# Kernel tuning notes

Hardware: AMD Instinct MI355X
Metric: run time of the kernel (lower is better)

Reference implementation:

```python
import jax, jax.numpy as jnp
import numpy as np

IN_NF, IN_EF, OUT_NF, H1, H2, H_IN = 16, 8, 16, 8, 8, 16
N_NODES, N_EDGES = 100000, 2000000


def _mlp(x, w1, b1, w2, b2):
    # Linear -> LeakyReLU(0.2) -> Linear
    return jax.nn.leaky_relu(x @ w1 + b1, negative_slope=0.2) @ w2 + b2


def setup_inputs() -> dict:
    key = jax.random.key(0)
    ks = jax.random.split(key, 20)
    d_in = 2 * IN_NF + IN_EF  # 40
    inp = {
        "nf": jax.random.normal(ks[0], (N_NODES, IN_NF), jnp.float32),
        "src_out": jax.random.randint(ks[1], (N_EDGES,), 0, N_NODES),
        "dst_out": jax.random.randint(ks[2], (N_EDGES,), 0, N_NODES),
        "nef_out": jax.random.normal(ks[3], (N_EDGES, IN_EF), jnp.float32),
        "src_in": jax.random.randint(ks[4], (N_EDGES,), 0, N_NODES),
        "dst_in": jax.random.randint(ks[5], (N_EDGES,), 0, N_NODES),
        "nef_in": jax.random.normal(ks[6], (N_EDGES, IN_EF), jnp.float32),
        # MLP_msg_o2i: (2*in_nf+in_ef) -> h_in -> out_nf
        "w_o2i1": jax.random.normal(ks[7], (d_in, H_IN), jnp.float32) * 0.1,
        "b_o2i1": jnp.zeros((H_IN,), jnp.float32),
        "w_o2i2": jax.random.normal(ks[8], (H_IN, OUT_NF), jnp.float32) * 0.1,
        "b_o2i2": jnp.zeros((OUT_NF,), jnp.float32),
        # MLP_msg_i2o: (2*in_nf+in_ef) -> h_in -> 1+h1+h2
        "w_i2o1": jax.random.normal(ks[9], (d_in, H_IN), jnp.float32) * 0.1,
        "b_i2o1": jnp.zeros((H_IN,), jnp.float32),
        "w_i2o2": jax.random.normal(ks[10], (H_IN, 1 + H1 + H2), jnp.float32) * 0.1,
        "b_i2o2": jnp.zeros((1 + H1 + H2,), jnp.float32),
        # MLP_reduce_o: (in_nf+h1+h2) -> h_in -> out_nf  (note: in_nf==out_nf here)
        "w_red1": jax.random.normal(ks[11], (OUT_NF + H1 + H2, H_IN), jnp.float32) * 0.1,
        "b_red1": jnp.zeros((H_IN,), jnp.float32),
        "w_red2": jax.random.normal(ks[12], (H_IN, OUT_NF), jnp.float32) * 0.1,
        "b_red2": jnp.zeros((OUT_NF,), jnp.float32),
    }
    return inp


def reference(nf, src_out, dst_out, nef_out, src_in, dst_in, nef_in,
              w_o2i1, b_o2i1, w_o2i2, b_o2i2,
              w_i2o1, b_i2o1, w_i2o2, b_i2o2,
              w_red1, b_red1, w_red2, b_red2):
    n = nf.shape[0]
    # --- update_all over 'net_out': edge gather-concat -> MLP -> scatter sum
    x_o = jnp.concatenate([nf[src_out], nf[dst_out], nef_out], axis=1)  # [E, 40]
    efi = _mlp(x_o, w_o2i1, b_o2i1, w_o2i2, b_o2i2)                      # [E, out_nf]
    new_nf = jax.ops.segment_sum(efi, dst_out, num_segments=n)           # overwrites 'new_nf'
    # --- apply_edges over 'net_in': gated messages
    x_i = jnp.concatenate([nf[src_in], nf[dst_in], nef_in], axis=1)      # [E, 40]
    m = _mlp(x_i, w_i2o1, b_i2o1, w_i2o2, b_i2o2)                        # [E, 1+h1+h2]
    k = jax.nn.sigmoid(m[:, :1])
    efo1 = m[:, 1:1 + H1] * k
    efo2 = m[:, 1 + H1:] * k
    # --- scatter sum / mean into dst nodes
    nfo1 = jax.ops.segment_sum(efo1, dst_in, num_segments=n)
    cnt = jax.ops.segment_sum(jnp.ones((dst_in.shape[0],), nf.dtype), dst_in, num_segments=n)
    nfo2 = jax.ops.segment_sum(efo2, dst_in, num_segments=n) / jnp.maximum(cnt, 1.0)[:, None]
    # --- apply_nodes only on net_in destination nodes; others keep new_nf
    reduced = _mlp(jnp.concatenate([new_nf, nfo1, nfo2], axis=1), w_red1, b_red1, w_red2, b_red2)
    has_in = (cnt > 0)[:, None]
    return jnp.where(has_in, reduced, new_nf)
```

## Files before the change

### kernel.cpp

```cpp
#include <hip/hip_runtime.h>
#include <math.h>

#define IN_NF 16
#define IN_EF 8
#define OUT_NF 16
#define H1 8
#define H2 8
#define H_IN 16
#define NT 4
#define SCAN_NB 128

typedef unsigned int uivec4 __attribute__((ext_vector_type(4)));

__device__ __forceinline__ unsigned int f2bf_bits(float f) {
    unsigned int u = __float_as_uint(f);
    u += 0x7FFFu + ((u >> 16) & 1u);
    return u >> 16;
}
__device__ __forceinline__ float bf_lo(unsigned int w) { return __uint_as_float(w << 16); }
__device__ __forceinline__ float bf_hi(unsigned int w) { return __uint_as_float(w & 0xFFFF0000u); }

__global__ __launch_bounds__(256) void k_pre(
    const float* __restrict__ nf, unsigned short* __restrict__ nf16, int n_nodes,
    const int* __restrict__ dst_out, const int* __restrict__ dst_in,
// ... 20 lines not shown
            atomicAdd(&curA[a.x], 1); atomicAdd(&curA[a.y], 1);
            atomicAdd(&curA[a.z], 1); atomicAdd(&curA[a.w], 1);
            int4 b = *(const int4*)(dst_in + i);
            atomicAdd(&curB[b.x], 1); atomicAdd(&curB[b.y], 1);
            atomicAdd(&curB[b.z], 1); atomicAdd(&curB[b.w], 1);
        } else {
            for (int e = i; e < n_edges; ++e) {
                atomicAdd(&curA[dst_out[e]], 1);
                atomicAdd(&curB[dst_in[e]], 1);
            }
        }
    }
}

__global__ __launch_bounds__(256) void k_scan_partial(
    const int* __restrict__ a0, const int* __restrict__ a1, int n,
    int* __restrict__ bsum)
{
    int arr = blockIdx.x >> 7;
    int blk = blockIdx.x & (SCAN_NB - 1);
    const int* a = arr ? a1 : a0;
    int chunk = (n + SCAN_NB - 1) / SCAN_NB;
    int beg = blk * chunk;
    int end = min(beg + chunk, n);
    int s = 0;
    for (int i = beg + threadIdx.x; i < end; i += 256) s += a[i];
    __shared__ int sm[256];
    int t = threadIdx.x;
    sm[t] = s;
    __syncthreads();
    for (int d = 128; d > 0; d >>= 1) {
        if (t < d) sm[t] += sm[t + d];
        __syncthreads();
    }
    if (t == 0) bsum[arr * SCAN_NB + blk] = sm[0];
}

__global__ __launch_bounds__(64) void k_scan_bsum(int* __restrict__ bsum)
{
    int arr = threadIdx.x;
    if (arr >= 2) return;
    int run = 0;
    for (int i = 0; i < SCAN_NB; ++i) {
        int v = bsum[arr * SCAN_NB + i];
        bsum[arr * SCAN_NB + i] = run;
        run += v;
    }
}

__global__ __launch_bounds__(256) void k_scan_final(
    int* __restrict__ a0, int* __restrict__ a1, int n,
    const int* __restrict__ bsum)
{
    int arr = blockIdx.x >> 7;
    int blk = blockIdx.x & (SCAN_NB - 1);
    int* a = arr ? a1 : a0;
    int chunk = (n + SCAN_NB - 1) / SCAN_NB;
    int beg = blk * chunk;
    int end = min(beg + chunk, n);
    int t = threadIdx.x;
    __shared__ int sm[256];
    __shared__ int carry_sm;
    if (t == 0) carry_sm = bsum[arr * SCAN_NB + blk];
    __syncthreads();
    for (int base = beg; base < end; base += 256) {
        int i = base + t;
        int v = (i < end) ? a[i] : 0;
        sm[t] = v;
        __syncthreads();
        for (int d = 1; d < 256; d <<= 1) {
            int u = (t >= d) ? sm[t - d] : 0;
            __syncthreads();
            sm[t] += u;
            __syncthreads();
        }
        int carry = carry_sm;
        if (i < end) a[i] = carry + sm[t] - v;
        __syncthreads();
        if (t == 0) carry_sm = carry + sm[255];
        __syncthreads();
    }
}

__global__ __launch_bounds__(256, 4) void k_edges_stream(
    const unsigned short* __restrict__ nf16,
    const int* __restrict__ srcA, const int* __restrict__ dstA,
    const float* __restrict__ nefA,
    const int* __restrict__ srcB, const int* __restrict__ dstB,
    const float* __restrict__ nefB,
    const float* __restrict__ W1A, const float* __restrict__ B1A,
    const float* __restrict__ W2A, const float* __restrict__ B2A,
    const float* __restrict__ W1B, const float* __restrict__ B1B,
    const float* __restrict__ W2B, const float* __restrict__ B2B,
    int* __restrict__ curA, int* __restrict__ curB,
    int* __restrict__ invA, int* __restrict__ invB,
    unsigned short* __restrict__ msgA, unsigned short* __restrict__ msgB,
    int n_edges, int nbe)
{
    bool isA = (int)blockIdx.x < nbe;
    int bid = isA ? (int)blockIdx.x : (int)blockIdx.x - nbe;
    int e = bid * 256 + (int)threadIdx.x;
    if (e >= n_edges) return;

    const int* src = isA ? srcA : srcB;
    const int* dst = isA ? dstA : dstB;
    const float* nef = isA ? nefA : nefB;
    const float* W1 = isA ? W1A : W1B;
    const float* B1 = isA ? B1A : B1B;
    int* cursor = isA ? curA : curB;
    int* inv = isA ? invA : invB;
    unsigned short* msg = isA ? msgA : msgB;

    int s = src[e];
    int d = dst[e];

    const uint4* pS = (const uint4*)(nf16 + (size_t)s * 16);
    uint4 Sa = pS[0], Sb = pS[1];
    const uint4* pD = (const uint4*)(nf16 + (size_t)d * 16);
    uint4 Da = pD[0], Db = pD[1];
    const float4* pN = (const float4*)(nef + (size_t)e * IN_EF);
    float4 Na = pN[0], Nb = pN[1];

    int slot = atomicAdd(&cursor[d], 1);

    float h[H_IN];
#pragma unroll
    for (int j = 0; j < H_IN; ++j) h[j] = B1[j];
    {
        unsigned int wS[8] = {Sa.x,Sa.y,Sa.z,Sa.w,Sb.x,Sb.y,Sb.z,Sb.w};
        unsigned int wD[8] = {Da.x,Da.y,Da.z,Da.w,Db.x,Db.y,Db.z,Db.w};
#pragma unroll
        for (int w = 0; w < 8; ++w) {
            float a0 = bf_lo(wS[w]), a1 = bf_hi(wS[w]);
            float b0 = bf_lo(wD[w]), b1 = bf_hi(wD[w]);
            const float* r0 = W1 + (2*w) * H_IN;
            const float* r1 = W1 + (2*w+1) * H_IN;
            const float* r2 = W1 + (IN_NF + 2*w) * H_IN;
            const float* r3 = W1 + (IN_NF + 2*w+1) * H_IN;
#pragma unroll
            for (int j = 0; j < H_IN; ++j) {
                h[j] = fmaf(a0, r0[j], h[j]);
                h[j] = fmaf(a1, r1[j], h[j]);
                h[j] = fmaf(b0, r2[j], h[j]);
                h[j] = fmaf(b1, r3[j], h[j]);
            }
        }
        float nv[8] = {Na.x,Na.y,Na.z,Na.w,Nb.x,Nb.y,Nb.z,Nb.w};
#pragma unroll
        for (int k = 0; k < IN_EF; ++k) {
            const float* r = W1 + (2*IN_NF + k) * H_IN;
            float a0 = nv[k];
#pragma unroll
            for (int j = 0; j < H_IN; ++j) h[j] = fmaf(a0, r[j], h[j]);
        }
    }
#pragma unroll
    for (int j = 0; j < H_IN; ++j) h[j] = (h[j] >= 0.f) ? h[j] : 0.2f * h[j];

    unsigned int w[8];
    if (isA) {
        float o[OUT_NF];
#pragma unroll
        for (int j = 0; j < OUT_NF; ++j) o[j] = B2A[j];
#pragma unroll
        for (int k = 0; k < H_IN; ++k) {
            float hk = h[k];
            const float* r = W2A + k * OUT_NF;
#pragma unroll
            for (int j = 0; j < OUT_NF; ++j) o[j] = fmaf(hk, r[j], o[j]);
        }
#pragma unroll
        for (int q = 0; q < 8; ++q)
            w[q] = f2bf_bits(o[2*q]) | (f2bf_bits(o[2*q+1]) << 16);
    } else {
        const int M = 1 + H1 + H2;
        float o[17];
#pragma unroll
        for (int j = 0; j < M; ++j) o[j] = B2B[j];
#pragma unroll
        for (int k = 0; k < H_IN; ++k) {
            float hk = h[k];
            const float* r = W2B + k * M;
#pragma unroll
            for (int j = 0; j < M; ++j) o[j] = fmaf(hk, r[j], o[j]);
        }
        float g = 1.f / (1.f + __expf(-o[0]));
#pragma unroll
        for (int q = 0; q < 8; ++q)
            w[q] = f2bf_bits(o[1+2*q] * g) | (f2bf_bits(o[2+2*q] * g) << 16);
    }

    uivec4* pm = (uivec4*)(msg + (size_t)e * 16);
    uivec4 v0 = {w[0], w[1], w[2], w[3]};
    uivec4 v1 = {w[4], w[5], w[6], w[7]};
    __builtin_nontemporal_store(v0, pm);
    __builtin_nontemporal_store(v1, pm + 1);
    inv[slot] = e;
}

__global__ __launch_bounds__(256, 4) void k_gather_ind(
    const int* __restrict__ curA, const int* __restrict__ curB,
    const int* __restrict__ invA, const int* __restrict__ invB,
    const unsigned short* __restrict__ msgA, const unsigned short* __restrict__ msgB,
    const float* __restrict__ w_red1, const float* __restrict__ b_red1,
    const float* __restrict__ w_red2, const float* __restrict__ b_red2,
    float* __restrict__ out, int n_nodes)
{
    int tid = blockIdx.x * blockDim.x + threadIdx.x;
    int node = tid >> 2;
    int t = tid & (NT - 1);
    if (node >= n_nodes) return;

    int begA = (node == 0) ? 0 : curA[node - 1];
    int endA = curA[node];
    int begB = (node == 0) ? 0 : curB[node - 1];
    int endB = curB[node];

    float accA[16], accB[16];
#pragma unroll
    for (int j = 0; j < 16; ++j) { accA[j] = 0.f; accB[j] = 0.f; }

    {
        int i = begA + t;
        int e = (i < endA) ? invA[i] : 0;
        while (i < endA) {
            int inext = i + NT;
            int enext = (inext < endA) ? invA[inext] : 0;
            const uint4* p = (const uint4*)(msgA + (size_t)e * 16);
            uint4 v0 = p[0], v1 = p[1];
            unsigned int w0=v0.x,w1=v0.y,w2=v0.z,w3=v0.w,w4=v1.x,w5=v1.y,w6=v1.z,w7=v1.w;
            accA[0]+=bf_lo(w0); accA[1]+=bf_hi(w0); accA[2]+=bf_lo(w1); accA[3]+=bf_hi(w1);
            accA[4]+=bf_lo(w2); accA[5]+=bf_hi(w2); accA[6]+=bf_lo(w3); accA[7]+=bf_hi(w3);
            accA[8]+=bf_lo(w4); accA[9]+=bf_hi(w4); accA[10]+=bf_lo(w5); accA[11]+=bf_hi(w5);
            accA[12]+=bf_lo(w6); accA[13]+=bf_hi(w6); accA[14]+=bf_lo(w7); accA[15]+=bf_hi(w7);
            i = inext; e = enext;
        }
    }
    {
        int i = begB + t;
        int e = (i < endB) ? invB[i] : 0;
        while (i < endB) {
            int inext = i + NT;
            int enext = (inext < endB) ? invB[inext] : 0;
            const uint4* p = (const uint4*)(msgB + (size_t)e * 16);
            uint4 v0 = p[0], v1 = p[1];
            unsigned int w0=v0.x,w1=v0.y,w2=v0.z,w3=v0.w,w4=v1.x,w5=v1.y,w6=v1.z,w7=v1.w;
            accB[0]+=bf_lo(w0); accB[1]+=bf_hi(w0); accB[2]+=bf_lo(w1); accB[3]+=bf_hi(w1);
            accB[4]+=bf_lo(w2); accB[5]+=bf_hi(w2); accB[6]+=bf_lo(w3); accB[7]+=bf_hi(w3);
            accB[8]+=bf_lo(w4); accB[9]+=bf_hi(w4); accB[10]+=bf_lo(w5); accB[11]+=bf_hi(w5);
            accB[12]+=bf_lo(w6); accB[13]+=bf_hi(w6); accB[14]+=bf_lo(w7); accB[15]+=bf_hi(w7);
            i = inext; e = enext;
        }
    }

#pragma unroll
    for (int mask = 1; mask < NT; mask <<= 1) {
#pragma unroll
        for (int j = 0; j < 16; ++j) {
            accA[j] += __shfl_xor(accA[j], mask);
            accB[j] += __shfl_xor(accB[j], mask);
        }
    }
    if (t != 0) return;

    int deg = endB - begB;
    float inv = 1.f / fmaxf((float)deg, 1.f);
    float x2[32];
#pragma unroll
    for (int j = 0; j < 16; ++j) x2[j] = accA[j];
#pragma unroll
    for (int j = 0; j < H1; ++j) x2[16 + j] = accB[j];
#pragma unroll
    for (int j = 0; j < H2; ++j) x2[16 + H1 + j] = accB[8 + j] * inv;

    float h[H_IN];
#pragma unroll
    for (int j = 0; j < H_IN; ++j) h[j] = b_red1[j];
#pragma unroll
    for (int k = 0; k < 32; ++k) {
        float xk = x2[k];
#pragma unroll
        for (int j = 0; j < H_IN; ++j) h[j] = fmaf(xk, w_red1[k * H_IN + j], h[j]);
    }
#pragma unroll
    for (int j = 0; j < H_IN; ++j) h[j] = (h[j] >= 0.f) ? h[j] : 0.2f * h[j];

    float o[OUT_NF];
#pragma unroll
    for (int j = 0; j < OUT_NF; ++j) o[j] = b_red2[j];
#pragma unroll
    for (int k = 0; k < H_IN; ++k) {
        float hk = h[k];
#pragma unroll
        for (int j = 0; j < OUT_NF; ++j) o[j] = fmaf(hk, w_red2[k * OUT_NF + j], o[j]);
    }

    bool has_in = (deg > 0);
    float4* po = (float4*)(out + (long)node * OUT_NF);
#pragma unroll
    for (int i = 0; i < 4; ++i) {
        float4 v;
        if (has_in) { v.x=o[4*i+0]; v.y=o[4*i+1]; v.z=o[4*i+2]; v.w=o[4*i+3]; }
        else        { v.x=accA[4*i+0]; v.y=accA[4*i+1]; v.z=accA[4*i+2]; v.w=accA[4*i+3]; }
        po[i] = v;
    }
}

__global__ __launch_bounds__(256, 4) void k_edges_csr(
    const unsigned short* __restrict__ nf16,
    const int* __restrict__ srcA, const int* __restrict__ dstA,
    const float* __restrict__ nefA,
    const int* __restrict__ srcB, const int* __restrict__ dstB,
    const float* __restrict__ nefB,
    const float* __restrict__ W1A, const float* __restrict__ B1A,
    const float* __restrict__ W2A, const float* __restrict__ B2A,
    const float* __restrict__ W1B, const float* __restrict__ B1B,
    const float* __restrict__ W2B, const float* __restrict__ B2B,
    int* __restrict__ curA, int* __restrict__ curB,
    unsigned short* __restrict__ msgA, unsigned short* __restrict__ msgB,
    int n_edges, int nbe)
{
    bool isA = (int)blockIdx.x < nbe;
    int bid = isA ? (int)blockIdx.x : (int)blockIdx.x - nbe;
    int e = bid * 256 + (int)threadIdx.x;
    if (e >= n_edges) return;

    const int* src = isA ? srcA : srcB;
    const int* dst = isA ? dstA : dstB;
    const float* nef = isA ? nefA : nefB;
    const float* W1 = isA ? W1A : W1B;
    const float* B1 = isA ? B1A : B1B;
    int* cursor = isA ? curA : curB;
    unsigned short* msg = isA ? msgA : msgB;

    int s = src[e];
    int d = dst[e];

    const uint4* pS = (const uint4*)(nf16 + (size_t)s * 16);
    uint4 Sa = pS[0], Sb = pS[1];
    const uint4* pD = (const uint4*)(nf16 + (size_t)d * 16);
    uint4 Da = pD[0], Db = pD[1];
    const float4* pN = (const float4*)(nef + (size_t)e * IN_EF);
    float4 Na = pN[0], Nb = pN[1];

    int slot = atomicAdd(&cursor[d], 1);

    float h[H_IN];
#pragma unroll
    for (int j = 0; j < H_IN; ++j) h[j] = B1[j];
    {
        unsigned int wS[8] = {Sa.x,Sa.y,Sa.z,Sa.w,Sb.x,Sb.y,Sb.z,Sb.w};
        unsigned int wD[8] = {Da.x,Da.y,Da.z,Da.w,Db.x,Db.y,Db.z,Db.w};
#pragma unroll
        for (int w = 0; w < 8; ++w) {
            float a0 = bf_lo(wS[w]), a1 = bf_hi(wS[w]);
            float b0 = bf_lo(wD[w]), b1 = bf_hi(wD[w]);
            const float* r0 = W1 + (2*w) * H_IN;
            const float* r1 = W1 + (2*w+1) * H_IN;
            const float* r2 = W1 + (IN_NF + 2*w) * H_IN;
            const float* r3 = W1 + (IN_NF + 2*w+1) * H_IN;
#pragma unroll
            for (int j = 0; j < H_IN; ++j) {
                h[j] = fmaf(a0, r0[j], h[j]);
                h[j] = fmaf(a1, r1[j], h[j]);
                h[j] = fmaf(b0, r2[j], h[j]);
                h[j] = fmaf(b1, r3[j], h[j]);
            }
        }
        float nv[8] = {Na.x,Na.y,Na.z,Na.w,Nb.x,Nb.y,Nb.z,Nb.w};
#pragma unroll
        for (int k = 0; k < IN_EF; ++k) {
            const float* r = W1 + (2*IN_NF + k) * H_IN;
            float a0 = nv[k];
#pragma unroll
            for (int j = 0; j < H_IN; ++j) h[j] = fmaf(a0, r[j], h[j]);
        }
    }
#pragma unroll
    for (int j = 0; j < H_IN; ++j) h[j] = (h[j] >= 0.f) ? h[j] : 0.2f * h[j];

    unsigned int w[8];
    if (isA) {
        float o[OUT_NF];
#pragma unroll
        for (int j = 0; j < OUT_NF; ++j) o[j] = B2A[j];
#pragma unroll
        for (int k = 0; k < H_IN; ++k) {
            float hk = h[k];
            const float* r = W2A + k * OUT_NF;
#pragma unroll
            for (int j = 0; j < OUT_NF; ++j) o[j] = fmaf(hk, r[j], o[j]);
        }
#pragma unroll
        for (int q = 0; q < 8; ++q)
            w[q] = f2bf_bits(o[2*q]) | (f2bf_bits(o[2*q+1]) << 16);
    } else {
        const int M = 1 + H1 + H2;
        float o[17];
#pragma unroll
        for (int j = 0; j < M; ++j) o[j] = B2B[j];
#pragma unroll
        for (int k = 0; k < H_IN; ++k) {
            float hk = h[k];
            const float* r = W2B + k * M;
#pragma unroll
            for (int j = 0; j < M; ++j) o[j] = fmaf(hk, r[j], o[j]);
        }
        float g = 1.f / (1.f + __expf(-o[0]));
#pragma unroll
        for (int q = 0; q < 8; ++q)
            w[q] = f2bf_bits(o[1+2*q] * g) | (f2bf_bits(o[2+2*q] * g) << 16);
    }

    uivec4* pm = (uivec4*)(msg + (size_t)slot * 16);
    uivec4 v0 = {w[0], w[1], w[2], w[3]};
    uivec4 v1 = {w[4], w[5], w[6], w[7]};
    __builtin_nontemporal_store(v0, pm);
    __builtin_nontemporal_store(v1, pm + 1);
}

__global__ __launch_bounds__(256, 4) void k_gather_csr(
    const int* __restrict__ curA, const int* __restrict__ curB,
    const unsigned short* __restrict__ msgA, const unsigned short* __restrict__ msgB,
    const float* __restrict__ w_red1, const float* __restrict__ b_red1,
    const float* __restrict__ w_red2, const float* __restrict__ b_red2,
    float* __restrict__ out, int n_nodes)
{
    int tid = blockIdx.x * blockDim.x + threadIdx.x;
    int node = tid >> 2;
    int t = tid & (NT - 1);
    if (node >= n_nodes) return;

    int begA = (node == 0) ? 0 : curA[node - 1];
    int endA = curA[node];
    int begB = (node == 0) ? 0 : curB[node - 1];
    int endB = curB[node];

    float accA[16], accB[16];
#pragma unroll
    for (int j = 0; j < 16; ++j) { accA[j] = 0.f; accB[j] = 0.f; }

    for (int i = begA + t; i < endA; i += NT) {
        const uint4* p = (const uint4*)(msgA + (size_t)i * 16);
        uint4 v0 = p[0], v1 = p[1];
        unsigned int w0=v0.x,w1=v0.y,w2=v0.z,w3=v0.w,w4=v1.x,w5=v1.y,w6=v1.z,w7=v1.w;
        accA[0]+=bf_lo(w0); accA[1]+=bf_hi(w0); accA[2]+=bf_lo(w1); accA[3]+=bf_hi(w1);
        accA[4]+=bf_lo(w2); accA[5]+=bf_hi(w2); accA[6]+=bf_lo(w3); accA[7]+=bf_hi(w3);
        accA[8]+=bf_lo(w4); accA[9]+=bf_hi(w4); accA[10]+=bf_lo(w5); accA[11]+=bf_hi(w5);
        accA[12]+=bf_lo(w6); accA[13]+=bf_hi(w6); accA[14]+=bf_lo(w7); accA[15]+=bf_hi(w7);
    }
    for (int i = begB + t; i < endB; i += NT) {
        const uint4* p = (const uint4*)(msgB + (size_t)i * 16);
        uint4 v0 = p[0], v1 = p[1];
        unsigned int w0=v0.x,w1=v0.y,w2=v0.z,w3=v0.w,w4=v1.x,w5=v1.y,w6=v1.z,w7=v1.w;
        accB[0]+=bf_lo(w0); accB[1]+=bf_hi(w0); accB[2]+=bf_lo(w1); accB[3]+=bf_hi(w1);
        accB[4]+=bf_lo(w2); accB[5]+=bf_hi(w2); accB[6]+=bf_lo(w3); accB[7]+=bf_hi(w3);
        accB[8]+=bf_lo(w4); accB[9]+=bf_hi(w4); accB[10]+=bf_lo(w5); accB[11]+=bf_hi(w5);
        accB[12]+=bf_lo(w6); accB[13]+=bf_hi(w6); accB[14]+=bf_lo(w7); accB[15]+=bf_hi(w7);
    }

#pragma unroll
    for (int mask = 1; mask < NT; mask <<= 1) {
#pragma unroll
        for (int j = 0; j < 16; ++j) {
            accA[j] += __shfl_xor(accA[j], mask);
            accB[j] += __shfl_xor(accB[j], mask);
        }
    }
    if (t != 0) return;

    int deg = endB - begB;
    float inv = 1.f / fmaxf((float)deg, 1.f);
    float x2[32];
#pragma unroll
    for (int j = 0; j < 16; ++j) x2[j] = accA[j];
#pragma unroll
    for (int j = 0; j < H1; ++j) x2[16 + j] = accB[j];
#pragma unroll
    for (int j = 0; j < H2; ++j) x2[16 + H1 + j] = accB[8 + j] * inv;

    float h[H_IN];
#pragma unroll
    for (int j = 0; j < H_IN; ++j) h[j] = b_red1[j];
#pragma unroll
    for (int k = 0; k < 32; ++k) {
        float xk = x2[k];
#pragma unroll
        for (int j = 0; j < H_IN; ++j) h[j] = fmaf(xk, w_red1[k * H_IN + j], h[j]);
    }
#pragma unroll
    for (int j = 0; j < H_IN; ++j) h[j] = (h[j] >= 0.f) ? h[j] : 0.2f * h[j];

    float o[OUT_NF];
#pragma unroll
    for (int j = 0; j < OUT_NF; ++j) o[j] = b_red2[j];
#pragma unroll
    for (int k = 0; k < H_IN; ++k) {
        float hk = h[k];
#pragma unroll
        for (int j = 0; j < OUT_NF; ++j) o[j] = fmaf(hk, w_red2[k * OUT_NF + j], o[j]);
    }

    bool has_in = (deg > 0);
    float4* po = (float4*)(out + (long)node * OUT_NF);
#pragma unroll
    for (int i = 0; i < 4; ++i) {
        float4 v;
        if (has_in) { v.x=o[4*i+0]; v.y=o[4*i+1]; v.z=o[4*i+2]; v.w=o[4*i+3]; }
        else        { v.x=accA[4*i+0]; v.y=accA[4*i+1]; v.z=accA[4*i+2]; v.w=accA[4*i+3]; }
        po[i] = v;
    }
}

extern "C" void kernel_launch(void* const* d_in, const int* in_sizes, int n_in,
                              void* d_out, int out_size, void* d_ws, size_t ws_size,
                              hipStream_t stream) {
    const float* nf      = (const float*)d_in[0];
    const int*   src_out = (const int*)d_in[1];
    const int*   dst_out = (const int*)d_in[2];
    const float* nef_out = (const float*)d_in[3];
    const int*   src_in  = (const int*)d_in[4];
    const int*   dst_in  = (const int*)d_in[5];
    const float* nef_in  = (const float*)d_in[6];
    const float* w_o2i1  = (const float*)d_in[7];
    const float* b_o2i1  = (const float*)d_in[8];
    const float* w_o2i2  = (const float*)d_in[9];
    const float* b_o2i2  = (const float*)d_in[10];
    const float* w_i2o1  = (const float*)d_in[11];
    const float* b_i2o1  = (const float*)d_in[12];
    const float* w_i2o2  = (const float*)d_in[13];
    const float* b_i2o2  = (const float*)d_in[14];
    const float* w_red1  = (const float*)d_in[15];
    const float* b_red1  = (const float*)d_in[16];
    const float* w_red2  = (const float*)d_in[17];
    const float* b_red2  = (const float*)d_in[18];

    int n_nodes = in_sizes[0] / IN_NF;
    int n_edges = in_sizes[1];
    float* out = (float*)d_out;

    dim3 blk(256);
    dim3 ngrid(((size_t)n_nodes * NT + 255) / 256);
    dim3 sgrid(2 * SCAN_NB);

    size_t off_bytes  = (size_t)2 * n_nodes * sizeof(int);
    size_t nf16_bytes = (size_t)n_nodes * 16 * sizeof(unsigned short);
    size_t inv_bytes  = (size_t)n_edges * sizeof(int);
    size_t msg_bytes  = (size_t)n_edges * 16 * sizeof(unsigned short);
    size_t need2 = off_bytes + nf16_bytes + 2 * inv_bytes + 2 * msg_bytes + 256;

    int nb_conv = (n_nodes + 255) / 256;
    int nb_hist = (n_edges / 4 + 256) / 256 + 1;
    dim3 pgrid(nb_conv + nb_hist);
    int nbe = (n_edges + 255) / 256;
    dim3 edge_grid(2 * nbe);

    if (ws_size >= need2) {
        int* curA = (int*)d_ws;
        int* curB = curA + n_nodes;
        unsigned short* nf16 = (unsigned short*)(curB + n_nodes);
        int* invA = (int*)(nf16 + (size_t)n_nodes * 16);
        int* invB = invA + n_edges;
        unsigned short* msgA = (unsigned short*)(invB + n_edges);
        unsigned short* msgB = msgA + (size_t)n_edges * 16;
        int* bsum = (int*)msgA;

        hipMemsetAsync(d_ws, 0, off_bytes, stream);
        k_pre<<<pgrid, blk, 0, stream>>>(nf, nf16, n_nodes, dst_out, dst_in,
                                         curA, curB, n_edges, nb_conv);
        k_scan_partial<<<sgrid, blk, 0, stream>>>(curA, curB, n_nodes, bsum);
        k_scan_bsum<<<dim3(1), dim3(64), 0, stream>>>(bsum);
        k_scan_final<<<sgrid, blk, 0, stream>>>(curA, curB, n_nodes, bsum);
        k_edges_stream<<<edge_grid, blk, 0, stream>>>(nf16,
                                               src_out, dst_out, nef_out,
                                               src_in, dst_in, nef_in,
                                               w_o2i1, b_o2i1, w_o2i2, b_o2i2,
                                               w_i2o1, b_i2o1, w_i2o2, b_i2o2,
                                               curA, curB, invA, invB,
                                               msgA, msgB, n_edges, nbe);
        k_gather_ind<<<ngrid, blk, 0, stream>>>(curA, curB, invA, invB,
                                            msgA, msgB,
                                            w_red1, b_red1, w_red2, b_red2,
                                            out, n_nodes);
    } else {
        int* curA = (int*)d_ws;
        int* curB = curA + n_nodes;
        unsigned short* nf16 = (unsigned short*)(curB + n_nodes);
        unsigned short* msgA = nf16 + (size_t)n_nodes * 16;
        unsigned short* msgB = msgA + (size_t)n_edges * 16;
        int* bsum = (int*)msgA;

        hipMemsetAsync(d_ws, 0, off_bytes, stream);
        k_pre<<<pgrid, blk, 0, stream>>>(nf, nf16, n_nodes, dst_out, dst_in,
                                         curA, curB, n_edges, nb_conv);
        k_scan_partial<<<sgrid, blk, 0, stream>>>(curA, curB, n_nodes, bsum);
        k_scan_bsum<<<dim3(1), dim3(64), 0, stream>>>(bsum);
        k_scan_final<<<sgrid, blk, 0, stream>>>(curA, curB, n_nodes, bsum);
        k_edges_csr<<<edge_grid, blk, 0, stream>>>(nf16,
                                               src_out, dst_out, nef_out,
                                               src_in, dst_in, nef_in,
                                               w_o2i1, b_o2i1, w_o2i2, b_o2i2,
                                               w_i2o1, b_i2o1, w_i2o2, b_i2o2,
                                               curA, curB, msgA, msgB,
                                               n_edges, nbe);
        k_gather_csr<<<ngrid, blk, 0, stream>>>(curA, curB, msgA, msgB,
                                            w_red1, b_red1, w_red2, b_red2,
                                            out, n_nodes);
    }
}
```

Before: 566.8 us.

## Compute edge MLPs per destination node, skipping per-edge message buffers

Replaces the edge-parallel MLP pass, which wrote bf16 messages for a later gather, with a lightweight permutation scatter followed by destination-node kernels. These walk each node's incoming edges, run the MLPs in place and accumulate the results directly. The destination-node part of the first layer and the second-layer bias are hoisted out of the per-edge loop. This removes the per-edge message write and reread, at the cost of random reads of src features and nef through the permutation and load imbalance across node degrees. The fallback path for small workspaces is dropped.

```diff
diff --git a/kernel.cpp b/kernel.cpp
--- a/kernel.cpp
+++ b/kernel.cpp
@@ -126,289 +126,85 @@
     }
 }
 
-__global__ __launch_bounds__(256, 4) void k_edges_stream(
+__global__ __launch_bounds__(256) void k_scatter(
+    const int* __restrict__ dst_out, const int* __restrict__ dst_in,
+    int* __restrict__ curA, int* __restrict__ curB,
+    int* __restrict__ permA, int* __restrict__ permB, int n_edges)
+{
+    int e = blockIdx.x * blockDim.x + threadIdx.x;
+    if (e >= n_edges) return;
+    int p0 = atomicAdd(&curA[dst_out[e]], 1);
+    permA[p0] = e;
+    int p1 = atomicAdd(&curB[dst_in[e]], 1);
+    permB[p1] = e;
+}
+
+__global__ __launch_bounds__(256, 4) void k_nodeA(
     const unsigned short* __restrict__ nf16,
-    const int* __restrict__ srcA, const int* __restrict__ dstA,
-    const float* __restrict__ nefA,
-    const int* __restrict__ srcB, const int* __restrict__ dstB,
-    const float* __restrict__ nefB,
-    const float* __restrict__ W1A, const float* __restrict__ B1A,
-    const float* __restrict__ W2A, const float* __restrict__ B2A,
-    const float* __restrict__ W1B, const float* __restrict__ B1B,
-    const float* __restrict__ W2B, const float* __restrict__ B2B,
-    int* __restrict__ curA, int* __restrict__ curB,
-    int* __restrict__ invA, int* __restrict__ invB,
-    unsigned short* __restrict__ msgA, unsigned short* __restrict__ msgB,
-    int n_edges, int nbe)
-{
-    bool isA = (int)blockIdx.x < nbe;
-    int bid = isA ? (int)blockIdx.x : (int)blockIdx.x - nbe;
-    int e = bid * 256 + (int)threadIdx.x;
-    if (e >= n_edges) return;
-
-    const int* src = isA ? srcA : srcB;
-    const int* dst = isA ? dstA : dstB;
-    const float* nef = isA ? nefA : nefB;
-    const float* W1 = isA ? W1A : W1B;
-    const float* B1 = isA ? B1A : B1B;
-    int* cursor = isA ? curA : curB;
-    int* inv = isA ? invA : invB;
-    unsigned short* msg = isA ? msgA : msgB;
-
-    int s = src[e];
-    int d = dst[e];
-
-    const uint4* pS = (const uint4*)(nf16 + (size_t)s * 16);
-    uint4 Sa = pS[0], Sb = pS[1];
-    const uint4* pD = (const uint4*)(nf16 + (size_t)d * 16);
-    uint4 Da = pD[0], Db = pD[1];
-    const float4* pN = (const float4*)(nef + (size_t)e * IN_EF);
-    float4 Na = pN[0], Nb = pN[1];
-
-    int slot = atomicAdd(&cursor[d], 1);
-
-    float h[H_IN];
-#pragma unroll
-    for (int j = 0; j < H_IN; ++j) h[j] = B1[j];
-    {
-        unsigned int wS[8] = {Sa.x,Sa.y,Sa.z,Sa.w,Sb.x,Sb.y,Sb.z,Sb.w};
-        unsigned int wD[8] = {Da.x,Da.y,Da.z,Da.w,Db.x,Db.y,Db.z,Db.w};
-#pragma unroll
-        for (int w = 0; w < 8; ++w) {
-            float a0 = bf_lo(wS[w]), a1 = bf_hi(wS[w]);
-            float b0 = bf_lo(wD[w]), b1 = bf_hi(wD[w]);
-            const float* r0 = W1 + (2*w) * H_IN;
-            const float* r1 = W1 + (2*w+1) * H_IN;
-            const float* r2 = W1 + (IN_NF + 2*w) * H_IN;
-            const float* r3 = W1 + (IN_NF + 2*w+1) * H_IN;
-#pragma unroll
-            for (int j = 0; j < H_IN; ++j) {
-                h[j] = fmaf(a0, r0[j], h[j]);
-                h[j] = fmaf(a1, r1[j], h[j]);
-                h[j] = fmaf(b0, r2[j], h[j]);
-                h[j] = fmaf(b1, r3[j], h[j]);
-            }
-        }
-        float nv[8] = {Na.x,Na.y,Na.z,Na.w,Nb.x,Nb.y,Nb.z,Nb.w};
-#pragma unroll
-        for (int k = 0; k < IN_EF; ++k) {
-            const float* r = W1 + (2*IN_NF + k) * H_IN;
-            float a0 = nv[k];
-#pragma unroll
-            for (int j = 0; j < H_IN; ++j) h[j] = fmaf(a0, r[j], h[j]);
-        }
-    }
-#pragma unroll
-    for (int j = 0; j < H_IN; ++j) h[j] = (h[j] >= 0.f) ? h[j] : 0.2f * h[j];
-
-    unsigned int w[8];
-    if (isA) {
-        float o[OUT_NF];
-#pragma unroll
-        for (int j = 0; j < OUT_NF; ++j) o[j] = B2A[j];
-#pragma unroll
-        for (int k = 0; k < H_IN; ++k) {
-            float hk = h[k];
-            const float* r = W2A + k * OUT_NF;
-#pragma unroll
-            for (int j = 0; j < OUT_NF; ++j) o[j] = fmaf(hk, r[j], o[j]);
-        }
-#pragma unroll
-        for (int q = 0; q < 8; ++q)
-            w[q] = f2bf_bits(o[2*q]) | (f2bf_bits(o[2*q+1]) << 16);
-    } else {
-        const int M = 1 + H1 + H2;
-        float o[17];
-#pragma unroll
-        for (int j = 0; j < M; ++j) o[j] = B2B[j];
-#pragma unroll
-        for (int k = 0; k < H_IN; ++k) {
-            float hk = h[k];
-            const float* r = W2B + k * M;
-#pragma unroll
-            for (int j = 0; j < M; ++j) o[j] = fmaf(hk, r[j], o[j]);
-        }
-        float g = 1.f / (1.f + __expf(-o[0]));
-#pragma unroll
-        for (int q = 0; q < 8; ++q)
-            w[q] = f2bf_bits(o[1+2*q] * g) | (f2bf_bits(o[2+2*q] * g) << 16);
-    }
-
-    uivec4* pm = (uivec4*)(msg + (size_t)e * 16);
-    uivec4 v0 = {w[0], w[1], w[2], w[3]};
-    uivec4 v1 = {w[4], w[5], w[6], w[7]};
-    __builtin_nontemporal_store(v0, pm);
-    __builtin_nontemporal_store(v1, pm + 1);
-    inv[slot] = e;
-}
-
-__global__ __launch_bounds__(256, 4) void k_gather_ind(
-    const int* __restrict__ curA, const int* __restrict__ curB,
-    const int* __restrict__ invA, const int* __restrict__ invB,
-    const unsigned short* __restrict__ msgA, const unsigned short* __restrict__ msgB,
-    const float* __restrict__ w_red1, const float* __restrict__ b_red1,
-    const float* __restrict__ w_red2, const float* __restrict__ b_red2,
-    float* __restrict__ out, int n_nodes)
+    const int* __restrict__ src, const float* __restrict__ nef,
+    const int* __restrict__ cur, const int* __restrict__ perm,
+    const float* __restrict__ W1, const float* __restrict__ B1,
+    const float* __restrict__ W2, const float* __restrict__ B2,
+    float* __restrict__ outA, int n_nodes)
 {
     int tid = blockIdx.x * blockDim.x + threadIdx.x;
     int node = tid >> 2;
     int t = tid & (NT - 1);
     if (node >= n_nodes) return;
 
-    int begA = (node == 0) ? 0 : curA[node - 1];
-    int endA = curA[node];
-    int begB = (node == 0) ? 0 : curB[node - 1];
-    int endB = curB[node];
-
-    float accA[16], accB[16];
-#pragma unroll
-    for (int j = 0; j < 16; ++j) { accA[j] = 0.f; accB[j] = 0.f; }
-
+    float hb[H_IN];
+#pragma unroll
+    for (int j = 0; j < H_IN; ++j) hb[j] = B1[j];
     {
-        int i = begA + t;
-        int e = (i < endA) ? invA[i] : 0;
-        while (i < endA) {
-            int inext = i + NT;
-            int enext = (inext < endA) ? invA[inext] : 0;
-            const uint4* p = (const uint4*)(msgA + (size_t)e * 16);
-            uint4 v0 = p[0], v1 = p[1];
-            unsigned int w0=v0.x,w1=v0.y,w2=v0.z,w3=v0.w,w4=v1.x,w5=v1.y,w6=v1.z,w7=v1.w;
-            accA[0]+=bf_lo(w0); accA[1]+=bf_hi(w0); accA[2]+=bf_lo(w1); accA[3]+=bf_hi(w1);
-            accA[4]+=bf_lo(w2); accA[5]+=bf_hi(w2); accA[6]+=bf_lo(w3); accA[7]+=bf_hi(w3);
-            accA[8]+=bf_lo(w4); accA[9]+=bf_hi(w4); accA[10]+=bf_lo(w5); accA[11]+=bf_hi(w5);
-            accA[12]+=bf_lo(w6); accA[13]+=bf_hi(w6); accA[14]+=bf_lo(w7); accA[15]+=bf_hi(w7);
-            i = inext; e = enext;
-        }
-    }
-    {
-        int i = begB + t;
-        int e = (i < endB) ? invB[i] : 0;
-        while (i < endB) {
-            int inext = i + NT;
-            int enext = (inext < endB) ? invB[inext] : 0;
-            const uint4* p = (const uint4*)(msgB + (size_t)e * 16);
-            uint4 v0 = p[0], v1 = p[1];
-            unsigned int w0=v0.x,w1=v0.y,w2=v0.z,w3=v0.w,w4=v1.x,w5=v1.y,w6=v1.z,w7=v1.w;
-            accB[0]+=bf_lo(w0); accB[1]+=bf_hi(w0); accB[2]+=bf_lo(w1); accB[3]+=bf_hi(w1);
-            accB[4]+=bf_lo(w2); accB[5]+=bf_hi(w2); accB[6]+=bf_lo(w3); accB[7]+=bf_hi(w3);
-            accB[8]+=bf_lo(w4); accB[9]+=bf_hi(w4); accB[10]+=bf_lo(w5); accB[11]+=bf_hi(w5);
-            accB[12]+=bf_lo(w6); accB[13]+=bf_hi(w6); accB[14]+=bf_lo(w7); accB[15]+=bf_hi(w7);
-            i = inext; e = enext;
-        }
-    }
-
-#pragma unroll
-    for (int mask = 1; mask < NT; mask <<= 1) {
-#pragma unroll
-        for (int j = 0; j < 16; ++j) {
-            accA[j] += __shfl_xor(accA[j], mask);
-            accB[j] += __shfl_xor(accB[j], mask);
-        }
-    }
-    if (t != 0) return;
-
-    int deg = endB - begB;
-    float inv = 1.f / fmaxf((float)deg, 1.f);
-    float x2[32];
-#pragma unroll
-    for (int j = 0; j < 16; ++j) x2[j] = accA[j];
-#pragma unroll
-    for (int j = 0; j < H1; ++j) x2[16 + j] = accB[j];
-#pragma unroll
-    for (int j = 0; j < H2; ++j) x2[16 + H1 + j] = accB[8 + j] * inv;
-
-    float h[H_IN];
-#pragma unroll
-    for (int j = 0; j < H_IN; ++j) h[j] = b_red1[j];
-#pragma unroll
-    for (int k = 0; k < 32; ++k) {
-        float xk = x2[k];
-#pragma unroll
-        for (int j = 0; j < H_IN; ++j) h[j] = fmaf(xk, w_red1[k * H_IN + j], h[j]);
-    }
-#pragma unroll
-    for (int j = 0; j < H_IN; ++j) h[j] = (h[j] >= 0.f) ? h[j] : 0.2f * h[j];
-
-    float o[OUT_NF];
-#pragma unroll
-    for (int j = 0; j < OUT_NF; ++j) o[j] = b_red2[j];
-#pragma unroll
-    for (int k = 0; k < H_IN; ++k) {
-        float hk = h[k];
-#pragma unroll
-        for (int j = 0; j < OUT_NF; ++j) o[j] = fmaf(hk, w_red2[k * OUT_NF + j], o[j]);
-    }
-
-    bool has_in = (deg > 0);
-    float4* po = (float4*)(out + (long)node * OUT_NF);
-#pragma unroll
-    for (int i = 0; i < 4; ++i) {
-        float4 v;
-        if (has_in) { v.x=o[4*i+0]; v.y=o[4*i+1]; v.z=o[4*i+2]; v.w=o[4*i+3]; }
-        else        { v.x=accA[4*i+0]; v.y=accA[4*i+1]; v.z=accA[4*i+2]; v.w=accA[4*i+3]; }
-        po[i] = v;
-    }
-}
-
-__global__ __launch_bounds__(256, 4) void k_edges_csr(
-    const unsigned short* __restrict__ nf16,
-    const int* __restrict__ srcA, const int* __restrict__ dstA,
-    const float* __restrict__ nefA,
-    const int* __restrict__ srcB, const int* __restrict__ dstB,
-    const float* __restrict__ nefB,
-    const float* __restrict__ W1A, const float* __restrict__ B1A,
-    const float* __restrict__ W2A, const float* __restrict__ B2A,
-    const float* __restrict__ W1B, const float* __restrict__ B1B,
-    const float* __restrict__ W2B, const float* __restrict__ B2B,
-    int* __restrict__ curA, int* __restrict__ curB,
-    unsigned short* __restrict__ msgA, unsigned short* __restrict__ msgB,
-    int n_edges, int nbe)
-{
-    bool isA = (int)blockIdx.x < nbe;
-    int bid = isA ? (int)blockIdx.x : (int)blockIdx.x - nbe;
-    int e = bid * 256 + (int)threadIdx.x;
-    if (e >= n_edges) return;
-
-    const int* src = isA ? srcA : srcB;
-    const int* dst = isA ? dstA : dstB;
-    const float* nef = isA ? nefA : nefB;
-    const float* W1 = isA ? W1A : W1B;
-    const float* B1 = isA ? B1A : B1B;
-    int* cursor = isA ? curA : curB;
-    unsigned short* msg = isA ? msgA : msgB;
-
-    int s = src[e];
-    int d = dst[e];
-
-    const uint4* pS = (const uint4*)(nf16 + (size_t)s * 16);
-    uint4 Sa = pS[0], Sb = pS[1];
-    const uint4* pD = (const uint4*)(nf16 + (size_t)d * 16);
-    uint4 Da = pD[0], Db = pD[1];
-    const float4* pN = (const float4*)(nef + (size_t)e * IN_EF);
-    float4 Na = pN[0], Nb = pN[1];
-
-    int slot = atomicAdd(&cursor[d], 1);
-
-    float h[H_IN];
-#pragma unroll
-    for (int j = 0; j < H_IN; ++j) h[j] = B1[j];
-    {
+        const uint4* pD = (const uint4*)(nf16 + (size_t)node * 16);
+        uint4 Da = pD[0], Db = pD[1];
+        unsigned int wD[8] = {Da.x,Da.y,Da.z,Da.w,Db.x,Db.y,Db.z,Db.w};
+#pragma unroll
+        for (int w = 0; w < 8; ++w) {
+            float b0 = bf_lo(wD[w]), b1 = bf_hi(wD[w]);
+            const float* r0 = W1 + (IN_NF + 2*w) * H_IN;
+            const float* r1 = W1 + (IN_NF + 2*w+1) * H_IN;
+#pragma unroll
+            for (int j = 0; j < H_IN; ++j) {
+                hb[j] = fmaf(b0, r0[j], hb[j]);
+                hb[j] = fmaf(b1, r1[j], hb[j]);
+            }
+        }
+    }
+
+    int beg = (node == 0) ? 0 : cur[node - 1];
+    int end = cur[node];
+
+    float acc[OUT_NF];
+#pragma unroll
+    for (int j = 0; j < OUT_NF; ++j) acc[j] = 0.f;
+    int local = 0;
+
+    int i = beg + t;
+    int e = (i < end) ? perm[i] : 0;
+    int s = (i < end) ? src[e] : 0;
+    while (i < end) {
+        int inext = i + NT;
+        int enext = (inext < end) ? perm[inext] : 0;
+        const uint4* pS = (const uint4*)(nf16 + (size_t)s * 16);
+        uint4 Sa = pS[0], Sb = pS[1];
+        const float4* pN = (const float4*)(nef + (size_t)e * IN_EF);
+        float4 Na = pN[0], Nb = pN[1];
+        int snext = (inext < end) ? src[enext] : 0;
+
+        float h[H_IN];
+#pragma unroll
+        for (int j = 0; j < H_IN; ++j) h[j] = hb[j];
         unsigned int wS[8] = {Sa.x,Sa.y,Sa.z,Sa.w,Sb.x,Sb.y,Sb.z,Sb.w};
-        unsigned int wD[8] = {Da.x,Da.y,Da.z,Da.w,Db.x,Db.y,Db.z,Db.w};
 #pragma unroll
         for (int w = 0; w < 8; ++w) {
             float a0 = bf_lo(wS[w]), a1 = bf_hi(wS[w]);
-            float b0 = bf_lo(wD[w]), b1 = bf_hi(wD[w]);
             const float* r0 = W1 + (2*w) * H_IN;
             const float* r1 = W1 + (2*w+1) * H_IN;
-            const float* r2 = W1 + (IN_NF + 2*w) * H_IN;
-            const float* r3 = W1 + (IN_NF + 2*w+1) * H_IN;
 #pragma unroll
             for (int j = 0; j < H_IN; ++j) {
                 h[j] = fmaf(a0, r0[j], h[j]);
                 h[j] = fmaf(a1, r1[j], h[j]);
-                h[j] = fmaf(b0, r2[j], h[j]);
-                h[j] = fmaf(b1, r3[j], h[j]);
             }
         }
         float nv[8] = {Na.x,Na.y,Na.z,Na.w,Nb.x,Nb.y,Nb.z,Nb.w};
@@ -419,140 +215,220 @@
 #pragma unroll
             for (int j = 0; j < H_IN; ++j) h[j] = fmaf(a0, r[j], h[j]);
         }
-    }
-#pragma unroll
-    for (int j = 0; j < H_IN; ++j) h[j] = (h[j] >= 0.f) ? h[j] : 0.2f * h[j];
-
-    unsigned int w[8];
-    if (isA) {
-        float o[OUT_NF];
-#pragma unroll
-        for (int j = 0; j < OUT_NF; ++j) o[j] = B2A[j];
+#pragma unroll
+        for (int j = 0; j < H_IN; ++j) h[j] = (h[j] >= 0.f) ? h[j] : 0.2f * h[j];
+
 #pragma unroll
         for (int k = 0; k < H_IN; ++k) {
             float hk = h[k];
-            const float* r = W2A + k * OUT_NF;
-#pragma unroll
-            for (int j = 0; j < OUT_NF; ++j) o[j] = fmaf(hk, r[j], o[j]);
-        }
-#pragma unroll
-        for (int q = 0; q < 8; ++q)
-            w[q] = f2bf_bits(o[2*q]) | (f2bf_bits(o[2*q+1]) << 16);
-    } else {
-        const int M = 1 + H1 + H2;
-        float o[17];
-#pragma unroll
-        for (int j = 0; j < M; ++j) o[j] = B2B[j];
-#pragma unroll
-        for (int k = 0; k < H_IN; ++k) {
-            float hk = h[k];
-            const float* r = W2B + k * M;
-#pragma unroll
-            for (int j = 0; j < M; ++j) o[j] = fmaf(hk, r[j], o[j]);
-        }
-        float g = 1.f / (1.f + __expf(-o[0]));
-#pragma unroll
-        for (int q = 0; q < 8; ++q)
-            w[q] = f2bf_bits(o[1+2*q] * g) | (f2bf_bits(o[2+2*q] * g) << 16);
-    }
-
-    uivec4* pm = (uivec4*)(msg + (size_t)slot * 16);
-    uivec4 v0 = {w[0], w[1], w[2], w[3]};
-    uivec4 v1 = {w[4], w[5], w[6], w[7]};
-    __builtin_nontemporal_store(v0, pm);
-    __builtin_nontemporal_store(v1, pm + 1);
-}
-
-__global__ __launch_bounds__(256, 4) void k_gather_csr(
-    const int* __restrict__ curA, const int* __restrict__ curB,
-    const unsigned short* __restrict__ msgA, const unsigned short* __restrict__ msgB,
-    const float* __restrict__ w_red1, const float* __restrict__ b_red1,
-    const float* __restrict__ w_red2, const float* __restrict__ b_red2,
-    float* __restrict__ out, int n_nodes)
+            const float* r = W2 + k * OUT_NF;
+#pragma unroll
+            for (int j = 0; j < OUT_NF; ++j) acc[j] = fmaf(hk, r[j], acc[j]);
+        }
+        ++local;
+        i = inext; e = enext; s = snext;
+    }
+    {
+        float lf = (float)local;
+#pragma unroll
+        for (int j = 0; j < OUT_NF; ++j) acc[j] = fmaf(lf, B2[j], acc[j]);
+    }
+
+#pragma unroll
+    for (int mask = 1; mask < NT; mask <<= 1)
+#pragma unroll
+        for (int j = 0; j < OUT_NF; ++j) acc[j] += __shfl_xor(acc[j], mask);
+
+    if (t != 0) return;
+    float4* po = (float4*)(outA + (size_t)node * OUT_NF);
+#pragma unroll
+    for (int q = 0; q < 4; ++q) {
+        float4 v; v.x = acc[4*q]; v.y = acc[4*q+1]; v.z = acc[4*q+2]; v.w = acc[4*q+3];
+        po[q] = v;
+    }
+}
+
+__global__ __launch_bounds__(256, 4) void k_nodeB(
+    const unsigned short* __restrict__ nf16,
+    const int* __restrict__ src, const float* __restrict__ nef,
+    const int* __restrict__ cur, const int* __restrict__ perm,
+    const float* __restrict__ W1, const float* __restrict__ B1,
+    const float* __restrict__ W2, const float* __restrict__ B2,
+    float* __restrict__ outB, int n_nodes)
 {
     int tid = blockIdx.x * blockDim.x + threadIdx.x;
     int node = tid >> 2;
     int t = tid & (NT - 1);
     if (node >= n_nodes) return;
 
-    int begA = (node == 0) ? 0 : curA[node - 1];
-    int endA = curA[node];
-    int begB = (node == 0) ? 0 : curB[node - 1];
-    int endB = curB[node];
-
-    float accA[16], accB[16];
-#pragma unroll
-    for (int j = 0; j < 16; ++j) { accA[j] = 0.f; accB[j] = 0.f; }
-
-    for (int i = begA + t; i < endA; i += NT) {
-        const uint4* p = (const uint4*)(msgA + (size_t)i * 16);
-        uint4 v0 = p[0], v1 = p[1];
-        unsigned int w0=v0.x,w1=v0.y,w2=v0.z,w3=v0.w,w4=v1.x,w5=v1.y,w6=v1.z,w7=v1.w;
-        accA[0]+=bf_lo(w0); accA[1]+=bf_hi(w0); accA[2]+=bf_lo(w1); accA[3]+=bf_hi(w1);
-        accA[4]+=bf_lo(w2); accA[5]+=bf_hi(w2); accA[6]+=bf_lo(w3); accA[7]+=bf_hi(w3);
-        accA[8]+=bf_lo(w4); accA[9]+=bf_hi(w4); accA[10]+=bf_lo(w5); accA[11]+=bf_hi(w5);
-        accA[12]+=bf_lo(w6); accA[13]+=bf_hi(w6); accA[14]+=bf_lo(w7); accA[15]+=bf_hi(w7);
-    }
-    for (int i = begB + t; i < endB; i += NT) {
-        const uint4* p = (const uint4*)(msgB + (size_t)i * 16);
-        uint4 v0 = p[0], v1 = p[1];
-        unsigned int w0=v0.x,w1=v0.y,w2=v0.z,w3=v0.w,w4=v1.x,w5=v1.y,w6=v1.z,w7=v1.w;
-        accB[0]+=bf_lo(w0); accB[1]+=bf_hi(w0); accB[2]+=bf_lo(w1); accB[3]+=bf_hi(w1);
-        accB[4]+=bf_lo(w2); accB[5]+=bf_hi(w2); accB[6]+=bf_lo(w3); accB[7]+=bf_hi(w3);
-        accB[8]+=bf_lo(w4); accB[9]+=bf_hi(w4); accB[10]+=bf_lo(w5); accB[11]+=bf_hi(w5);
-        accB[12]+=bf_lo(w6); accB[13]+=bf_hi(w6); accB[14]+=bf_lo(w7); accB[15]+=bf_hi(w7);
+    float hb[H_IN];
+#pragma unroll
+    for (int j = 0; j < H_IN; ++j) hb[j] = B1[j];
+    {
+        const uint4* pD = (const uint4*)(nf16 + (size_t)node * 16);
+        uint4 Da = pD[0], Db = pD[1];
+        unsigned int wD[8] = {Da.x,Da.y,Da.z,Da.w,Db.x,Db.y,Db.z,Db.w};
+#pragma unroll
+        for (int w = 0; w < 8; ++w) {
+            float b0 = bf_lo(wD[w]), b1 = bf_hi(wD[w]);
+            const float* r0 = W1 + (IN_NF + 2*w) * H_IN;
+            const float* r1 = W1 + (IN_NF + 2*w+1) * H_IN;
+#pragma unroll
+            for (int j = 0; j < H_IN; ++j) {
+                hb[j] = fmaf(b0, r0[j], hb[j]);
+                hb[j] = fmaf(b1, r1[j], hb[j]);
+            }
+        }
+    }
+
+    int beg = (node == 0) ? 0 : cur[node - 1];
+    int end = cur[node];
+    const int M = 1 + H1 + H2;
+
+    float acc1[H1], acc2[H2];
+#pragma unroll
+    for (int j = 0; j < H1; ++j) acc1[j] = 0.f;
+#pragma unroll
+    for (int j = 0; j < H2; ++j) acc2[j] = 0.f;
+
+    int i = beg + t;
+    int e = (i < end) ? perm[i] : 0;
+    int s = (i < end) ? src[e] : 0;
+    while (i < end) {
+        int inext = i + NT;
+        int enext = (inext < end) ? perm[inext] : 0;
+        const uint4* pS = (const uint4*)(nf16 + (size_t)s * 16);
+        uint4 Sa = pS[0], Sb = pS[1];
+        const float4* pN = (const float4*)(nef + (size_t)e * IN_EF);
+        float4 Na = pN[0], Nb = pN[1];
+        int snext = (inext < end) ? src[enext] : 0;
+
+        float h[H_IN];
+#pragma unroll
+        for (int j = 0; j < H_IN; ++j) h[j] = hb[j];
+        unsigned int wS[8] = {Sa.x,Sa.y,Sa.z,Sa.w,Sb.x,Sb.y,Sb.z,Sb.w};
+#pragma unroll
+        for (int w = 0; w < 8; ++w) {
+            float a0 = bf_lo(wS[w]), a1 = bf_hi(wS[w]);
+            const float* r0 = W1 + (2*w) * H_IN;
+            const float* r1 = W1 + (2*w+1) * H_IN;
+#pragma unroll
+            for (int j = 0; j < H_IN; ++j) {
+                h[j] = fmaf(a0, r0[j], h[j]);
+                h[j] = fmaf(a1, r1[j], h[j]);
+            }
+        }
+        float nv[8] = {Na.x,Na.y,Na.z,Na.w,Nb.x,Nb.y,Nb.z,Nb.w};
+#pragma unroll
+        for (int k = 0; k < IN_EF; ++k) {
+            const float* r = W1 + (2*IN_NF + k) * H_IN;
+            float a0 = nv[k];
+#pragma unroll
+            for (int j = 0; j < H_IN; ++j) h[j] = fmaf(a0, r[j], h[j]);
+        }
+#pragma unroll
+        for (int j = 0; j < H_IN; ++j) h[j] = (h[j] >= 0.f) ? h[j] : 0.2f * h[j];
+
+        float o[17];
+#pragma unroll
+        for (int j = 0; j < M; ++j) o[j] = B2[j];
+#pragma unroll
+        for (int k = 0; k < H_IN; ++k) {
+            float hk = h[k];
+            const float* r = W2 + k * M;
+#pragma unroll
+            for (int j = 0; j < M; ++j) o[j] = fmaf(hk, r[j], o[j]);
+        }
+        float g = 1.f / (1.f + __expf(-o[0]));
+#pragma unroll
+        for (int j = 0; j < H1; ++j) acc1[j] = fmaf(o[1 + j], g, acc1[j]);
+#pragma unroll
+        for (int j = 0; j < H2; ++j) acc2[j] = fmaf(o[1 + H1 + j], g, acc2[j]);
+
+        i = inext; e = enext; s = snext;
     }
 
 #pragma unroll
     for (int mask = 1; mask < NT; mask <<= 1) {
 #pragma unroll
-        for (int j = 0; j < 16; ++j) {
-            accA[j] += __shfl_xor(accA[j], mask);
-            accB[j] += __shfl_xor(accB[j], mask);
-        }
+        for (int j = 0; j < H1; ++j) acc1[j] += __shfl_xor(acc1[j], mask);
+#pragma unroll
+        for (int j = 0; j < H2; ++j) acc2[j] += __shfl_xor(acc2[j], mask);
     }
     if (t != 0) return;
-
-    int deg = endB - begB;
+    float4* po = (float4*)(outB + (size_t)node * 16);
+    float4 v0; v0.x = acc1[0]; v0.y = acc1[1]; v0.z = acc1[2]; v0.w = acc1[3];
+    float4 v1; v1.x = acc1[4]; v1.y = acc1[5]; v1.z = acc1[6]; v1.w = acc1[7];
+    float4 v2; v2.x = acc2[0]; v2.y = acc2[1]; v2.z = acc2[2]; v2.w = acc2[3];
+    float4 v3; v3.x = acc2[4]; v3.y = acc2[5]; v3.z = acc2[6]; v3.w = acc2[7];
+    po[0] = v0; po[1] = v1; po[2] = v2; po[3] = v3;
+}
+
+__global__ __launch_bounds__(256) void k_final(
+    const float* __restrict__ wsA, const float* __restrict__ wsB,
+    const int* __restrict__ curB,
+    const float* __restrict__ W1, const float* __restrict__ B1,
+    const float* __restrict__ W2, const float* __restrict__ B2,
+    float* __restrict__ out, int n_nodes)
+{
+    int node = blockIdx.x * blockDim.x + threadIdx.x;
+    if (node >= n_nodes) return;
+
+    int beg = (node == 0) ? 0 : curB[node - 1];
+    int end = curB[node];
+    int deg = end - beg;
     float inv = 1.f / fmaxf((float)deg, 1.f);
+
     float x2[32];
-#pragma unroll
-    for (int j = 0; j < 16; ++j) x2[j] = accA[j];
-#pragma unroll
-    for (int j = 0; j < H1; ++j) x2[16 + j] = accB[j];
-#pragma unroll
-    for (int j = 0; j < H2; ++j) x2[16 + H1 + j] = accB[8 + j] * inv;
+    const float4* pa = (const float4*)(wsA + (size_t)node * 16);
+#pragma unroll
+    for (int q = 0; q < 4; ++q) {
+        float4 v = pa[q];
+        x2[4*q+0] = v.x; x2[4*q+1] = v.y; x2[4*q+2] = v.z; x2[4*q+3] = v.w;
+    }
+    const float4* pb = (const float4*)(wsB + (size_t)node * 16);
+#pragma unroll
+    for (int q = 0; q < 2; ++q) {
+        float4 v = pb[q];
+        x2[16+4*q+0] = v.x; x2[16+4*q+1] = v.y; x2[16+4*q+2] = v.z; x2[16+4*q+3] = v.w;
+    }
+#pragma unroll
+    for (int q = 0; q < 2; ++q) {
+        float4 v = pb[2 + q];
+        x2[24+4*q+0] = v.x * inv; x2[24+4*q+1] = v.y * inv;
+        x2[24+4*q+2] = v.z * inv; x2[24+4*q+3] = v.w * inv;
+    }
 
     float h[H_IN];
 #pragma unroll
-    for (int j = 0; j < H_IN; ++j) h[j] = b_red1[j];
+    for (int j = 0; j < H_IN; ++j) h[j] = B1[j];
 #pragma unroll
     for (int k = 0; k < 32; ++k) {
         float xk = x2[k];
 #pragma unroll
-        for (int j = 0; j < H_IN; ++j) h[j] = fmaf(xk, w_red1[k * H_IN + j], h[j]);
+        for (int j = 0; j < H_IN; ++j) h[j] = fmaf(xk, W1[k * H_IN + j], h[j]);
     }
 #pragma unroll
     for (int j = 0; j < H_IN; ++j) h[j] = (h[j] >= 0.f) ? h[j] : 0.2f * h[j];
 
     float o[OUT_NF];
 #pragma unroll
-    for (int j = 0; j < OUT_NF; ++j) o[j] = b_red2[j];
+    for (int j = 0; j < OUT_NF; ++j) o[j] = B2[j];
 #pragma unroll
     for (int k = 0; k < H_IN; ++k) {
         float hk = h[k];
 #pragma unroll
-        for (int j = 0; j < OUT_NF; ++j) o[j] = fmaf(hk, w_red2[k * OUT_NF + j], o[j]);
+        for (int j = 0; j < OUT_NF; ++j) o[j] = fmaf(hk, W2[k * OUT_NF + j], o[j]);
     }
 
     bool has_in = (deg > 0);
-    float4* po = (float4*)(out + (long)node * OUT_NF);
-#pragma unroll
-    for (int i = 0; i < 4; ++i) {
+    float4* po = (float4*)(out + (size_t)node * OUT_NF);
+#pragma unroll
+    for (int q = 0; q < 4; ++q) {
         float4 v;
-        if (has_in) { v.x=o[4*i+0]; v.y=o[4*i+1]; v.z=o[4*i+2]; v.w=o[4*i+3]; }
-        else        { v.x=accA[4*i+0]; v.y=accA[4*i+1]; v.z=accA[4*i+2]; v.w=accA[4*i+3]; }
-        po[i] = v;
+        if (has_in) { v.x=o[4*q]; v.y=o[4*q+1]; v.z=o[4*q+2]; v.w=o[4*q+3]; }
+        else        { v.x=x2[4*q]; v.y=x2[4*q+1]; v.z=x2[4*q+2]; v.w=x2[4*q+3]; }
+        po[q] = v;
     }
 }
 
@@ -584,30 +460,30 @@
     float* out = (float*)d_out;
 
     dim3 blk(256);
+    dim3 egrid((n_edges + 255) / 256);
     dim3 ngrid(((size_t)n_nodes * NT + 255) / 256);
+    dim3 cgrid((n_nodes + 255) / 256);
     dim3 sgrid(2 * SCAN_NB);
 
     size_t off_bytes  = (size_t)2 * n_nodes * sizeof(int);
     size_t nf16_bytes = (size_t)n_nodes * 16 * sizeof(unsigned short);
-    size_t inv_bytes  = (size_t)n_edges * sizeof(int);
-    size_t msg_bytes  = (size_t)n_edges * 16 * sizeof(unsigned short);
-    size_t need2 = off_bytes + nf16_bytes + 2 * inv_bytes + 2 * msg_bytes + 256;
+    size_t perm_bytes = (size_t)n_edges * sizeof(int);
+    size_t acc_bytes  = (size_t)n_nodes * 16 * sizeof(float);
+    size_t need_new = off_bytes + nf16_bytes + 2 * perm_bytes + 2 * acc_bytes + 256;
 
     int nb_conv = (n_nodes + 255) / 256;
     int nb_hist = (n_edges / 4 + 256) / 256 + 1;
     dim3 pgrid(nb_conv + nb_hist);
-    int nbe = (n_edges + 255) / 256;
-    dim3 edge_grid(2 * nbe);
-
-    if (ws_size >= need2) {
+
+    if (ws_size >= need_new) {
         int* curA = (int*)d_ws;
         int* curB = curA + n_nodes;
         unsigned short* nf16 = (unsigned short*)(curB + n_nodes);
-        int* invA = (int*)(nf16 + (size_t)n_nodes * 16);
-        int* invB = invA + n_edges;
-        unsigned short* msgA = (unsigned short*)(invB + n_edges);
-        unsigned short* msgB = msgA + (size_t)n_edges * 16;
-        int* bsum = (int*)msgA;
+        int* permA = (int*)(nf16 + (size_t)n_nodes * 16);
+        int* permB = permA + n_edges;
+        float* wsA = (float*)(permB + n_edges);
+        float* wsB = wsA + (size_t)n_nodes * 16;
+        int* bsum = permA;
 
         hipMemsetAsync(d_ws, 0, off_bytes, stream);
         k_pre<<<pgrid, blk, 0, stream>>>(nf, nf16, n_nodes, dst_out, dst_in,
@@ -615,40 +491,16 @@
         k_scan_partial<<<sgrid, blk, 0, stream>>>(curA, curB, n_nodes, bsum);
         k_scan_bsum<<<dim3(1), dim3(64), 0, stream>>>(bsum);
         k_scan_final<<<sgrid, blk, 0, stream>>>(curA, curB, n_nodes, bsum);
-        k_edges_stream<<<edge_grid, blk, 0, stream>>>(nf16,
-                                               src_out, dst_out, nef_out,
-                                               src_in, dst_in, nef_in,
-                                               w_o2i1, b_o2i1, w_o2i2, b_o2i2,
-                                               w_i2o1, b_i2o1, w_i2o2, b_i2o2,
-                                               curA, curB, invA, invB,
-                                               msgA, msgB, n_edges, nbe);
-        k_gather_ind<<<ngrid, blk, 0, stream>>>(curA, curB, invA, invB,
-                                            msgA, msgB,
-                                            w_red1, b_red1, w_red2, b_red2,
-                                            out, n_nodes);
-    } else {
-        int* curA = (int*)d_ws;
-        int* curB = curA + n_nodes;
-        unsigned short* nf16 = (unsigned short*)(curB + n_nodes);
-        unsigned short* msgA = nf16 + (size_t)n_nodes * 16;
-        unsigned short* msgB = msgA + (size_t)n_edges * 16;
-        int* bsum = (int*)msgA;
-
-        hipMemsetAsync(d_ws, 0, off_bytes, stream);
-        k_pre<<<pgrid, blk, 0, stream>>>(nf, nf16, n_nodes, dst_out, dst_in,
-                                         curA, curB, n_edges, nb_conv);
-        k_scan_partial<<<sgrid, blk, 0, stream>>>(curA, curB, n_nodes, bsum);
-        k_scan_bsum<<<dim3(1), dim3(64), 0, stream>>>(bsum);
-        k_scan_final<<<sgrid, blk, 0, stream>>>(curA, curB, n_nodes, bsum);
-        k_edges_csr<<<edge_grid, blk, 0, stream>>>(nf16,
-                                               src_out, dst_out, nef_out,
-                                               src_in, dst_in, nef_in,
-                                               w_o2i1, b_o2i1, w_o2i2, b_o2i2,
-                                               w_i2o1, b_i2o1, w_i2o2, b_i2o2,
-                                               curA, curB, msgA, msgB,
-                                               n_edges, nbe);
-        k_gather_csr<<<ngrid, blk, 0, stream>>>(curA, curB, msgA, msgB,
-                                            w_red1, b_red1, w_red2, b_red2,
-                                            out, n_nodes);
-    }
-}
+        k_scatter<<<egrid, blk, 0, stream>>>(dst_out, dst_in, curA, curB,
+                                             permA, permB, n_edges);
+        k_nodeA<<<ngrid, blk, 0, stream>>>(nf16, src_out, nef_out, curA, permA,
+                                           w_o2i1, b_o2i1, w_o2i2, b_o2i2,
+                                           wsA, n_nodes);
+        k_nodeB<<<ngrid, blk, 0, stream>>>(nf16, src_in, nef_in, curB, permB,
+                                           w_i2o1, b_i2o1, w_i2o2, b_i2o2,
+                                           wsB, n_nodes);
+        k_final<<<cgrid, blk, 0, stream>>>(wsA, wsB, curB,
+                                           w_red1, b_red1, w_red2, b_red2,
+                                           out, n_nodes);
+    }
+}
```

Result: slower. 1.332 ms (+135.0%).
